# Performance work log

Hardware: AMD Instinct MI355X
Metric: run time of the kernel (lower is better)

Reference implementation:

```python
import jax, jax.numpy as jnp
import numpy as np

B, N, T, D = 32, 19, 2048, 128
TOP_K = 3
THRESHOLD = 1e-4
TEMPERATURE = 0.1


def setup_inputs() -> dict:
    key = jax.random.key(0)
    features = jax.random.normal(key, (B, N, T, D), dtype=jnp.float32)
    return {"features": features}


def reference(features):
    b, n, t, d = features.shape
    # (B, N, T, D) -> (B*T, N, D)
    f = features.transpose(0, 2, 1, 3).reshape(b * t, n, d)
    # cosine similarity (F.normalize uses eps=1e-12 on the norm)
    norm = jnp.linalg.norm(f, axis=-1, keepdims=True)
    fn = f / jnp.maximum(norm, 1e-12)
    adj = jnp.einsum('bnd,bmd->bnm', fn, fn) / TEMPERATURE
    adj = jax.nn.softmax(adj, axis=-1)
    # top-k sparsification along last dim
    vals, idx = jax.lax.top_k(adj, TOP_K)
    adj = jnp.put_along_axis(jnp.zeros_like(adj), idx, vals, axis=-1, inplace=False)
    # threshold pruning
    adj = jnp.where(adj > THRESHOLD, adj, jnp.zeros_like(adj))
    # symmetrize
    adj = (adj + adj.transpose(0, 2, 1)) * 0.5
    return adj.reshape(b, t, n, n)
```

## Files before the change

### kernel.cpp

```cpp
#include <hip/hip_runtime.h>
#include <math.h>

namespace {

constexpr int kB = 32;
constexpr int kN = 19;
constexpr int kT = 2048;
constexpr int kD = 128;

constexpr int TILES = 32;
constexpr int TPT   = 10;
constexpr int BDIM  = TILES * TPT;
constexpr int KC    = 16;
constexpr int SROW  = kN * KC;
constexpr int CHUNK_F4 = TILES * kN * (KC / 4);

constexpr int RPAD  = 21;
constexpr int TSTR  = 400;

constexpr float kTempInv = 10.0f;
constexpr float kThresh  = 1e-4f;

__global__ __launch_bounds__(BDIM, 2)
void fused_graph_kernel(const float* __restrict__ feat, float* __restrict__ out)
{
    __shared__ float smem[TILES * TSTR];
    __shared__ float sInv[TILES * 20];

    const int tid = threadIdx.x;
    const int tl  = tid / TPT;
    const int sub = tid - tl * TPT;
    const int bi    = (sub >= 4) + (sub >= 7) + (sub >= 9);
    const int start = bi * 4 - (bi * (bi - 1)) / 2;
    const int bj    = bi + (sub - start);

    const int gt0 = blockIdx.x * TILES;
    const int b0  = gt0 >> 11;
    const int t0  = gt0 & (kT - 1);

    const float* blkBase = feat + ((size_t)b0 * kN * kT + (size_t)t0) * kD;

    int ar[5], bc[5];
#pragma unroll
    for (int r = 0; r < 5; ++r) { ar[r] = bi * 5 + r; if (ar[r] > kN - 1) ar[r] = kN - 1; }
#pragma unroll
    for (int c = 0; c < 5; ++c) { bc[c] = bj * 5 + c; if (bc[c] > kN - 1) bc[c] = kN - 1; }

    float acc[5][5];
#pragma unroll
    for (int r = 0; r < 5; ++r)
#pragma unroll
        for (int c = 0; c < 5; ++c) acc[r][c] = 0.f;

    for (int kc = 0; kc < kD; kc += KC) {
        for (int q = tid; q < CHUNK_F4; q += BDIM) {
            const int d4 = q & 3;
            const int t  = (q >> 2) & (TILES - 1);
            const int n  = q >> 7;
            const float4 v = *(const float4*)(blkBase + ((size_t)n << 18) + ((size_t)t << 7) + kc + d4 * 4);
            *(float4*)(&smem[t * SROW + n * KC + d4 * 4]) = v;
        }
        __syncthreads();

        const float* base = &smem[tl * SROW];
#pragma unroll
        for (int s0 = 0; s0 < 4; ++s0) {
            const int s = (s0 + sub) & 3;
            float4 ra[5], cb[5];
#pragma unroll
            for (int r = 0; r < 5; ++r)
                ra[r] = *(const float4*)(base + ar[r] * KC + s * 4);
            if (bi == bj) {
#pragma unroll
                for (int c = 0; c < 5; ++c) cb[c] = ra[c];
            } else {
#pragma unroll
                for (int c = 0; c < 5; ++c)
                    cb[c] = *(const float4*)(base + bc[c] * KC + s * 4);
            }
#pragma unroll
            for (int r = 0; r < 5; ++r)
#pragma unroll
                for (int c = 0; c < 5; ++c) {
                    acc[r][c] = fmaf(ra[r].x, cb[c].x, acc[r][c]);
                    acc[r][c] = fmaf(ra[r].y, cb[c].y, acc[r][c]);
                    acc[r][c] = fmaf(ra[r].z, cb[c].z, acc[r][c]);
                    acc[r][c] = fmaf(ra[r].w, cb[c].w, acc[r][c]);
                }
        }
        __syncthreads();
    }

    {
        float* g = &smem[tl * TSTR];
#pragma unroll
        for (int r = 0; r < 5; ++r) {
            const int i = bi * 5 + r;
#pragma unroll
            for (int c = 0; c < 5; ++c) {
                const int j = bj * 5 + c;
                if (i < kN && j < kN) {
                    g[i * RPAD + j] = acc[r][c];
                    if (i != j) g[j * RPAD + i] = acc[r][c];
                }
            }
        }
    }
    __syncthreads();

    for (int q = tid; q < TILES * kN; q += BDIM) {
        const int tt = q / kN;
        const int i  = q - tt * kN;
        const float nrm = sqrtf(smem[tt * TSTR + i * RPAD + i]);
        sInv[tt * 20 + i] = 1.0f / fmaxf(nrm, 1e-12f);
    }
    __syncthreads();

    for (int q = tid; q < TILES * kN; q += BDIM) {
        const int tt = q / kN;
        const int i  = q - tt * kN;
        float* row = &smem[tt * TSTR + i * RPAD];
        const float* invp = &sInv[tt * 20];
        const float si = invp[i] * kTempInv;

        float l[kN];
        float m = -3.0e38f;
#pragma unroll
        for (int j = 0; j < kN; ++j) {
            const float g = row[j] * si * invp[j];
            l[j] = g;
            m = fmaxf(m, g);
        }
        float ssum = 0.f;
#pragma unroll
        for (int j = 0; j < kN; ++j) {
            const float e = __expf(l[j] - m);
            l[j] = e;
            ssum += e;
        }
        const float rs = 1.0f / ssum;
#pragma unroll
        for (int j = 0; j < kN; ++j) l[j] *= rs;

        int k1 = 0; float v1 = -1.f;
#pragma unroll
        for (int j = 0; j < kN; ++j) if (l[j] > v1) { v1 = l[j]; k1 = j; }
        int k2 = -1; float v2 = -1.f;
#pragma unroll
        for (int j = 0; j < kN; ++j) if (j != k1 && l[j] > v2) { v2 = l[j]; k2 = j; }
        int k3 = -1; float v3 = -1.f;
#pragma unroll
        for (int j = 0; j < kN; ++j) if (j != k1 && j != k2 && l[j] > v3) { v3 = l[j]; k3 = j; }

#pragma unroll
        for (int j = 0; j < kN; ++j) {
            const float p = l[j];
            const bool keep = (j == k1 || j == k2 || j == k3) && (p > kThresh);
            row[j] = keep ? p : 0.f;
        }
    }
    __syncthreads();

    float* ob = out + (size_t)gt0 * (kN * kN);
    for (int q = tid; q < TILES * kN * kN; q += BDIM) {
        const int tt = q / (kN * kN);
        const int r  = q - tt * (kN * kN);
        const int i  = r / kN;
        const int j  = r - i * kN;
        const float v = 0.5f * (smem[tt * TSTR + i * RPAD + j] +
                                smem[tt * TSTR + j * RPAD + i]);
        ob[q] = v;
    }
}

}

extern "C" void kernel_launch(void* const* d_in, const int* in_sizes, int n_in,
                              void* d_out, int out_size, void* d_ws, size_t ws_size,
                              hipStream_t stream)
{
    const float* feat = (const float*)d_in[0];
    float* out = (float*)d_out;
    dim3 grid((kB * kT) / TILES);
    dim3 block(BDIM);
    hipLaunchKernelGGL(fused_graph_kernel, grid, block, 0, stream, feat, out);
}
```

Baseline: 1.065 ms.

## Shrink blocks to a single wavefront handling six timesteps each

Blocks shrink from 320 threads covering 32 timesteps to one 64-lane wavefront covering 6 timesteps. The grid becomes the ceiling of the timestep count over 6, with clamped global indexing and a bounded store for the partial last block. The aim is a smaller shared-memory footprint per block, more resident blocks, and cheaper barriers inside a single wave. In exchange, 4 of the 64 lanes sit idle, there are many more blocks, and each block gets less load parallelism and less reuse per load.

```diff
diff --git a/kernel.cpp b/kernel.cpp
--- a/kernel.cpp
+++ b/kernel.cpp
@@ -8,9 +8,9 @@
 constexpr int kT = 2048;
 constexpr int kD = 128;
 
-constexpr int TILES = 32;
+constexpr int TILES = 6;
 constexpr int TPT   = 10;
-constexpr int BDIM  = TILES * TPT;
+constexpr int BDIM  = 64;
 constexpr int KC    = 16;
 constexpr int SROW  = kN * KC;
 constexpr int CHUNK_F4 = TILES * kN * (KC / 4);
@@ -18,27 +18,29 @@
 constexpr int RPAD  = 21;
 constexpr int TSTR  = 400;
 
+constexpr int NT    = kB * kT;
+constexpr int NGRID = (NT + TILES - 1) / TILES;
+
 constexpr float kTempInv = 10.0f;
 constexpr float kThresh  = 1e-4f;
 
-__global__ __launch_bounds__(BDIM, 2)
+__global__ __launch_bounds__(BDIM, 4)
 void fused_graph_kernel(const float* __restrict__ feat, float* __restrict__ out)
 {
-    __shared__ float smem[TILES * TSTR];
-    __shared__ float sInv[TILES * 20];
+    __shared__ float smem[TILES * TSTR + TILES * 20];
 
-    const int tid = threadIdx.x;
-    const int tl  = tid / TPT;
-    const int sub = tid - tl * TPT;
+    const int lane = threadIdx.x;
+    int tl = lane / TPT;
+    const int sub = lane - tl * TPT;
+    const bool laneValid = (tl < TILES);
+    if (!laneValid) tl = TILES - 1;
+
     const int bi    = (sub >= 4) + (sub >= 7) + (sub >= 9);
     const int start = bi * 4 - (bi * (bi - 1)) / 2;
     const int bj    = bi + (sub - start);
 
     const int gt0 = blockIdx.x * TILES;
-    const int b0  = gt0 >> 11;
-    const int t0  = gt0 & (kT - 1);
-
-    const float* blkBase = feat + ((size_t)b0 * kN * kT + (size_t)t0) * kD;
+    const int vT  = (NT - gt0 < TILES) ? (NT - gt0) : TILES;
 
     int ar[5], bc[5];
 #pragma unroll
@@ -53,11 +55,15 @@
         for (int c = 0; c < 5; ++c) acc[r][c] = 0.f;
 
     for (int kc = 0; kc < kD; kc += KC) {
-        for (int q = tid; q < CHUNK_F4; q += BDIM) {
+        for (int q = lane; q < CHUNK_F4; q += BDIM) {
             const int d4 = q & 3;
-            const int t  = (q >> 2) & (TILES - 1);
-            const int n  = q >> 7;
-            const float4 v = *(const float4*)(blkBase + ((size_t)n << 18) + ((size_t)t << 7) + kc + d4 * 4);
+            const int r  = q >> 2;
+            const int t  = r % TILES;
+            const int n  = r / TILES;
+            int g = gt0 + t;
+            if (g > NT - 1) g = NT - 1;
+            const size_t flat = (((size_t)(g >> 11) * kN + n) << 11) + (size_t)(g & (kT - 1));
+            const float4 v = *(const float4*)(feat + (flat << 7) + kc + (d4 << 2));
             *(float4*)(&smem[t * SROW + n * KC + d4 * 4]) = v;
         }
         __syncthreads();
@@ -99,7 +105,7 @@
 #pragma unroll
             for (int c = 0; c < 5; ++c) {
                 const int j = bj * 5 + c;
-                if (i < kN && j < kN) {
+                if (laneValid && i < kN && j < kN) {
                     g[i * RPAD + j] = acc[r][c];
                     if (i != j) g[j * RPAD + i] = acc[r][c];
                 }
@@ -108,7 +114,8 @@
     }
     __syncthreads();
 
-    for (int q = tid; q < TILES * kN; q += BDIM) {
+    float* sInv = &smem[TILES * TSTR];
+    for (int q = lane; q < TILES * kN; q += BDIM) {
         const int tt = q / kN;
         const int i  = q - tt * kN;
         const float nrm = sqrtf(smem[tt * TSTR + i * RPAD + i]);
@@ -116,7 +123,7 @@
     }
     __syncthreads();
 
-    for (int q = tid; q < TILES * kN; q += BDIM) {
+    for (int q = lane; q < TILES * kN; q += BDIM) {
         const int tt = q / kN;
         const int i  = q - tt * kN;
         float* row = &smem[tt * TSTR + i * RPAD];
@@ -162,7 +169,8 @@
     __syncthreads();
 
     float* ob = out + (size_t)gt0 * (kN * kN);
-    for (int q = tid; q < TILES * kN * kN; q += BDIM) {
+    const int qMax = vT * (kN * kN);
+    for (int q = lane; q < qMax; q += BDIM) {
         const int tt = q / (kN * kN);
         const int r  = q - tt * (kN * kN);
         const int i  = r / kN;
@@ -181,7 +189,7 @@
 {
     const float* feat = (const float*)d_in[0];
     float* out = (float*)d_out;
-    dim3 grid((kB * kT) / TILES);
+    dim3 grid(NGRID);
     dim3 block(BDIM);
     hipLaunchKernelGGL(fused_graph_kernel, grid, block, 0, stream, feat, out);
 }
```

Result: slower. 1.617 ms (+51.8%).
